# Kernel tuning notes

Measured on AMD Instinct MI355X. Metric: run time of the kernel, lower is better.

## Reference

```python
import jax, jax.numpy as jnp
import numpy as np

# Winograd F(2x2, 3x3) transform matrices
B = jnp.array([[1.0, 0.0, 0.0, 0.0],
               [0.0, 1.0, -1.0, 1.0],
               [-1.0, 1.0, 1.0, 0.0],
               [0.0, 0.0, 0.0, -1.0]], dtype=jnp.float32)
G = jnp.array([[1.0, 0.0, 0.0],
               [0.5, 0.5, 0.5],
               [0.5, -0.5, 0.5],
               [0.0, 0.0, 1.0]], dtype=jnp.float32)
A = jnp.array([[1.0, 0.0],
               [1.0, 1.0],
               [1.0, -1.0],
               [0.0, -1.0]], dtype=jnp.float32)

PADDING = 1


def setup_inputs() -> dict:
    key = jax.random.key(0)
    k1, k2 = jax.random.split(key)
    x = jax.random.normal(k1, (16, 128, 56, 56), dtype=jnp.float32)
    kernel = jax.random.normal(k2, (128, 128, 3, 3), dtype=jnp.float32) * 0.05
    return {"x": x, "kernel": kernel}


def _winograd_fwd(x, kernel):
    # Pad input
    x = jnp.pad(x, ((0, 0), (0, 0), (PADDING, PADDING), (PADDING, PADDING)))
    N, C, H, W = x.shape
    a, overlap, m = 4, 2, 2  # tile size, stride, output tile
    Th = (H - a) // overlap + 1
    Tw = (W - a) // overlap + 1
    H_out, W_out = H - 2, W - 2

    # Filter transform: U = G @ g @ G^T  -> (K, C, 4, 4)
    U = jnp.einsum('ij,kcjl,ml->kcim', G, kernel, G)

    # Extract overlapping 4x4 tiles with stride 2: (N, C, Th, Tw, 4, 4)
    ii = (jnp.arange(Th) * overlap)[:, None] + jnp.arange(a)[None, :]  # (Th, 4)
    jj = (jnp.arange(Tw) * overlap)[:, None] + jnp.arange(a)[None, :]  # (Tw, 4)
    d = x[:, :, ii]               # (N, C, Th, 4, W)
    d = d[:, :, :, :, jj]         # (N, C, Th, 4, Tw, 4)
    d = d.transpose(0, 1, 2, 4, 3, 5)  # (N, C, Th, Tw, 4, 4)

    # Input transform: V = B^T @ d @ B
    V = jnp.einsum('ji,nchwjk,kl->nchwil', B, d, B)  # (N, C, Th, Tw, 4, 4)

    # Elementwise multiply + channel reduction: (N, K, Th, Tw, 4, 4)
    M = jnp.einsum('kcij,nchwij->nkhwij', U, V)

    # Output transform: Y_tile = A^T @ M @ A -> (N, K, Th, Tw, 2, 2)
    Yt = jnp.einsum('ji,nkhwjl,lm->nkhwim', A, M, A)

    # Reassemble tiles into (N, K, H_out, W_out)
    Y = Yt.transpose(0, 1, 2, 4, 3, 5).reshape(N, Yt.shape[1], H_out, W_out)
    return Y


def reference(x, kernel):
    return _winograd_fwd(x, kernel)
```

## Files before the change

### kernel.cpp

```cpp
#include <hip/hip_runtime.h>
#include <hip/hip_bf16.h>

typedef __attribute__((ext_vector_type(8))) short bf16x8;
typedef __attribute__((ext_vector_type(4))) float f32x4;

#define CC 128
#define KK 128
#define HH 56
#define WW 56
#define HW (HH * WW)

#define XP_OFF (512 * 1024)

__device__ __forceinline__ unsigned short f2bf(float f) {
  unsigned int u = __builtin_bit_cast(unsigned int, f);
  u += 0x7FFFu + ((u >> 16) & 1u);
  return (unsigned short)(u >> 16);
}

__device__ __forceinline__ void gload_lds16(const void* g, void* l) {
  __builtin_amdgcn_global_load_lds((__attribute__((address_space(1))) void*)g,
                                   (__attribute__((address_space(3))) void*)l,
                                   16, 0, 0);
}

__global__ void prepack_kernel(const float* __restrict__ x,
                               unsigned short* __restrict__ xp) {
  int idx = blockIdx.x * 256 + threadIdx.x;
  int w = idx % 66;
  int q = idx / 66;
  int cp = q & 15;
  int r = q >> 4;
  int h = r % 58;
  int n = r / 58;
  bool ok = (h >= 1) && (h <= 56) && (w >= 1) && (w <= 56);
  const float* src = x + ((size_t)(n * CC + cp * 8) * HH + (h - 1)) * WW + (w - 1);
  unsigned short o[8];
#pragma unroll
  for (int ci = 0; ci < 8; ++ci) {
    float v = ok ? src[(size_t)ci * HW] : 0.f;
    o[ci] = f2bf(v);
  }
  *(bf16x8*)(xp + (size_t)idx * 8) = *(bf16x8*)o;
}

__global__ void wtrans_kernel(const float* __restrict__ kin,
                              unsigned short* __restrict__ wt) {
  int e = blockIdx.x * 256 + threadIdx.x;
  int j = e & 7;
  int k = (e >> 3) & 127;
  int part = (e >> 10) & 3;
  int step = e >> 12;
  int rs = step >> 2;
  int cs = step & 3;
  int c = cs * 32 + part * 8 + j;
  wt[e] = f2bf(kin[(k * CC + c) * 9 + rs]);
}

__global__ __launch_bounds__(256, 3) void conv_kernel(
    const unsigned short* __restrict__ xp, const unsigned short* __restrict__ wt,
    float* __restrict__ out) {
  __shared__ __align__(16) unsigned char xs[3 * 16384];

  const int tid = threadIdx.x;
  const int lane = tid & 63;
  const int wv = tid >> 6;
  const int wm = wv >> 1;
  const int wn = wv & 1;

  const int wg = ((blockIdx.x & 7) * 56) + (blockIdx.x >> 3);
  const int n = wg / 28;
  const int hp = wg - n * 28;
  const int h0 = hp * 2;

  const unsigned char* xpb = (const unsigned char*)xp;
  const unsigned char* wtb = (const unsigned char*)wt;

  auto issue = [&](int t, int wr) {
    const int rs = t >> 2;
    const int cs = t & 3;
    const int fr = (rs * 11) >> 5;
    const int fs = rs - fr * 3;
    unsigned char* dst = xs + wr * 16384;
    const size_t rowcell = ((size_t)(n * 58 + h0 + fr) * 16 + cs * 4 + wv) * 66 + fs;
    gload_lds16(xpb + (rowcell + lane) * 16, dst + wv * 2048 + lane * 16);
    gload_lds16(xpb + (rowcell + 16 * 66 + lane) * 16,
                dst + wv * 2048 + 1024 + lane * 16);
    const unsigned char* bs = wtb + (size_t)t * 8192 + wv * 2048 + lane * 16;
    gload_lds16(bs, dst + 8192 + wv * 2048 + lane * 16);
    gload_lds16(bs + 1024, dst + 8192 + wv * 2048 + 1024 + lane * 16);
  };

  issue(0, 0);
  issue(1, 1);

  f32x4 acc[4][4] = {};
  const int fo = (lane >> 4) * 2048 + (lane & 15) * 16;

  int rd = 0, wr = 2;
#pragma unroll 1
  for (int t = 0; t < 36; ++t) {
    if (t < 35)
      asm volatile("s_waitcnt vmcnt(4)" ::: "memory");
    else
      asm volatile("s_waitcnt vmcnt(0)" ::: "memory");
    __builtin_amdgcn_s_barrier();

    if (t < 34) issue(t + 2, wr);

    const unsigned char* buf = xs + rd * 16384;
    bf16x8 Af[4], Bf[4];
#pragma unroll
    for (int am = 0; am < 4; ++am)
      Af[am] = *(const bf16x8*)(buf + fo + (wm * 64 + am * 16) * 16);
#pragma unroll
    for (int bn = 0; bn < 4; ++bn)
      Bf[bn] = *(const bf16x8*)(buf + 8192 + fo + (wn * 64 + bn * 16) * 16);

    __builtin_amdgcn_s_setprio(1);
#pragma unroll
    for (int am = 0; am < 4; ++am)
#pragma unroll
      for (int bn = 0; bn < 4; ++bn)
        acc[am][bn] = __builtin_amdgcn_mfma_f32_16x16x32_bf16(
            Af[am], Bf[bn], acc[am][bn], 0, 0, 0);
    __builtin_amdgcn_s_setprio(0);

    rd = (rd == 2) ? 0 : rd + 1;
    wr = (wr == 2) ? 0 : wr + 1;
  }

  const int h = h0 + wm;
  const int q4 = (lane >> 4) << 2;
#pragma unroll
  for (int am = 0; am < 4; ++am) {
    const int w0 = am * 16 + q4;
    if (w0 < WW) {
#pragma unroll
      for (int bn = 0; bn < 4; ++bn) {
        const int k = wn * 64 + bn * 16 + (lane & 15);
        float* op = out + ((size_t)(n * KK + k) * HH + h) * WW + w0;
        *(f32x4*)op = acc[am][bn];
      }
    }
  }
}

extern "C" void kernel_launch(void* const* d_in, const int* in_sizes, int n_in,
                              void* d_out, int out_size, void* d_ws, size_t ws_size,
                              hipStream_t stream) {
  const float* x = (const float*)d_in[0];
  const float* kin = (const float*)d_in[1];
  float* out = (float*)d_out;
  unsigned short* wt = (unsigned short*)d_ws;
  unsigned short* xp = (unsigned short*)((char*)d_ws + XP_OFF);

  hipLaunchKernelGGL(prepack_kernel, dim3(3828), dim3(256), 0, stream, x, xp);
  hipLaunchKernelGGL(wtrans_kernel, dim3(576), dim3(256), 0, stream, kin, wt);
  hipLaunchKernelGGL(conv_kernel, dim3(448), dim3(256), 0, stream, xp, wt, out);
}
```

Measured before the change: 40.33 us.

## Split conv tiles by output-channel half, pack two rows into M, merge prep kernels

The conv workgroup drops from 4 waves to 2 and covers 64 output channels instead of 128. Its 128-row M tile now packs both output rows (112 pixels) instead of padding each row to 64, so fewer MFMA rows are wasted, and the grid doubles to 896 blocks. The LDS pipeline moves from 3 to 4 stages with 3 loads in flight and smaller buffers. The input prepack and weight transform are merged into one launch to save a kernel launch. The risks are duplicated activation loads across the two channel halves and fewer waves per block to hide latency.

```diff
diff --git a/kernel.cpp b/kernel.cpp
--- a/kernel.cpp
+++ b/kernel.cpp
@@ -11,6 +11,8 @@
 #define HW (HH * WW)
 
 #define XP_OFF (512 * 1024)
+#define BUFSZ 12288
+#define ROWB (16 * 66 * 16)
 
 __device__ __forceinline__ unsigned short f2bf(float f) {
   unsigned int u = __builtin_bit_cast(unsigned int, f);
@@ -24,98 +26,117 @@
                                    16, 0, 0);
 }
 
-__global__ void prepack_kernel(const float* __restrict__ x,
-                               unsigned short* __restrict__ xp) {
-  int idx = blockIdx.x * 256 + threadIdx.x;
-  int w = idx % 66;
-  int q = idx / 66;
-  int cp = q & 15;
-  int r = q >> 4;
-  int h = r % 58;
-  int n = r / 58;
-  bool ok = (h >= 1) && (h <= 56) && (w >= 1) && (w <= 56);
-  const float* src = x + ((size_t)(n * CC + cp * 8) * HH + (h - 1)) * WW + (w - 1);
-  unsigned short o[8];
+__global__ void prep_kernel(const float* __restrict__ x,
+                            const float* __restrict__ kin,
+                            unsigned short* __restrict__ xp,
+                            unsigned short* __restrict__ wt) {
+  int b = blockIdx.x;
+  if (b < 3828) {
+    int idx = b * 256 + threadIdx.x;
+    int w = idx % 66;
+    int q = idx / 66;
+    int cp = q & 15;
+    int r = q >> 4;
+    int h = r % 58;
+    int n = r / 58;
+    bool ok = (h >= 1) && (h <= 56) && (w >= 1) && (w <= 56);
+    const float* src =
+        x + ((size_t)(n * CC + cp * 8) * HH + (h - 1)) * WW + (w - 1);
+    unsigned short o[8];
 #pragma unroll
-  for (int ci = 0; ci < 8; ++ci) {
-    float v = ok ? src[(size_t)ci * HW] : 0.f;
-    o[ci] = f2bf(v);
+    for (int ci = 0; ci < 8; ++ci) {
+      float v = ok ? src[(size_t)ci * HW] : 0.f;
+      o[ci] = f2bf(v);
+    }
+    *(bf16x8*)(xp + (size_t)idx * 8) = *(bf16x8*)o;
+  } else {
+    int e = (b - 3828) * 256 + threadIdx.x;
+    int j = e & 7;
+    int l = (e >> 3) & 63;
+    int p = (e >> 9) & 3;
+    int kn = (e >> 11) & 1;
+    int t = e >> 12;
+    int rs = t >> 2;
+    int cs = t & 3;
+    int k = kn * 64 + l;
+    int c = cs * 32 + p * 8 + j;
+    wt[e] = f2bf(kin[(k * CC + c) * 9 + rs]);
   }
-  *(bf16x8*)(xp + (size_t)idx * 8) = *(bf16x8*)o;
 }
 
-__global__ void wtrans_kernel(const float* __restrict__ kin,
-                              unsigned short* __restrict__ wt) {
-  int e = blockIdx.x * 256 + threadIdx.x;
-  int j = e & 7;
-  int k = (e >> 3) & 127;
-  int part = (e >> 10) & 3;
-  int step = e >> 12;
-  int rs = step >> 2;
-  int cs = step & 3;
-  int c = cs * 32 + part * 8 + j;
-  wt[e] = f2bf(kin[(k * CC + c) * 9 + rs]);
-}
-
-__global__ __launch_bounds__(256, 3) void conv_kernel(
+__global__ __launch_bounds__(128, 2) void conv_kernel(
     const unsigned short* __restrict__ xp, const unsigned short* __restrict__ wt,
     float* __restrict__ out) {
-  __shared__ __align__(16) unsigned char xs[3 * 16384];
+  __shared__ __align__(16) unsigned char xs[4 * BUFSZ];
 
   const int tid = threadIdx.x;
   const int lane = tid & 63;
   const int wv = tid >> 6;
-  const int wm = wv >> 1;
-  const int wn = wv & 1;
 
-  const int wg = ((blockIdx.x & 7) * 56) + (blockIdx.x >> 3);
-  const int n = wg / 28;
-  const int hp = wg - n * 28;
+  const int b = blockIdx.x;
+  const int wg = (b & 7) * 112 + (b >> 3);
+  const int kn = wg & 1;
+  const int mh = wg >> 1;
+  const int hp = mh % 28;
+  const int n = mh / 28;
   const int h0 = hp * 2;
 
   const unsigned char* xpb = (const unsigned char*)xp;
   const unsigned char* wtb = (const unsigned char*)wt;
 
-  auto issue = [&](int t, int wr) {
+  int offA0, offA1;
+  {
+    int dr = (lane >= 56) ? 1 : 0;
+    offA0 = dr * ROWB + (lane - 56 * dr) * 16;
+    offA1 = (lane < 48) ? (ROWB + (8 + lane) * 16)
+                        : (57 * 16);
+  }
+
+  auto issue = [&](int t, unsigned char* dst) {
     const int rs = t >> 2;
     const int cs = t & 3;
     const int fr = (rs * 11) >> 5;
     const int fs = rs - fr * 3;
-    unsigned char* dst = xs + wr * 16384;
-    const size_t rowcell = ((size_t)(n * 58 + h0 + fr) * 16 + cs * 4 + wv) * 66 + fs;
-    gload_lds16(xpb + (rowcell + lane) * 16, dst + wv * 2048 + lane * 16);
-    gload_lds16(xpb + (rowcell + 16 * 66 + lane) * 16,
-                dst + wv * 2048 + 1024 + lane * 16);
-    const unsigned char* bs = wtb + (size_t)t * 8192 + wv * 2048 + lane * 16;
-    gload_lds16(bs, dst + 8192 + wv * 2048 + lane * 16);
-    gload_lds16(bs + 1024, dst + 8192 + wv * 2048 + 1024 + lane * 16);
+#pragma unroll
+    for (int pi = 0; pi < 2; ++pi) {
+      const int p = wv * 2 + pi;
+      const size_t ab =
+          (((size_t)(n * 58 + h0 + fr) * 16 + (cs * 4 + p)) * 66 + fs) * 16;
+      gload_lds16(xpb + ab + offA0, dst + p * 2048 + lane * 16);
+      gload_lds16(xpb + ab + offA1, dst + p * 2048 + 1024 + lane * 16);
+      gload_lds16(wtb + (((t * 2 + kn) * 4 + p) << 10) + lane * 16,
+                  dst + 8192 + p * 1024 + lane * 16);
+    }
   };
 
-  issue(0, 0);
-  issue(1, 1);
+  issue(0, xs);
+  issue(1, xs + BUFSZ);
+  issue(2, xs + 2 * BUFSZ);
 
   f32x4 acc[4][4] = {};
   const int fo = (lane >> 4) * 2048 + (lane & 15) * 16;
+  const int fob = (lane >> 4) * 1024 + (lane & 15) * 16;
 
-  int rd = 0, wr = 2;
 #pragma unroll 1
   for (int t = 0; t < 36; ++t) {
-    if (t < 35)
-      asm volatile("s_waitcnt vmcnt(4)" ::: "memory");
+    if (t < 34)
+      asm volatile("s_waitcnt vmcnt(12)" ::: "memory");
+    else if (t == 34)
+      asm volatile("s_waitcnt vmcnt(6)" ::: "memory");
     else
       asm volatile("s_waitcnt vmcnt(0)" ::: "memory");
     __builtin_amdgcn_s_barrier();
 
-    if (t < 34) issue(t + 2, wr);
+    if (t < 33) issue(t + 3, xs + ((t + 3) & 3) * BUFSZ);
 
-    const unsigned char* buf = xs + rd * 16384;
+    const unsigned char* buf = xs + (t & 3) * BUFSZ;
     bf16x8 Af[4], Bf[4];
 #pragma unroll
     for (int am = 0; am < 4; ++am)
-      Af[am] = *(const bf16x8*)(buf + fo + (wm * 64 + am * 16) * 16);
+      Af[am] = *(const bf16x8*)(buf + fo + (wv * 64 + am * 16) * 16);
 #pragma unroll
     for (int bn = 0; bn < 4; ++bn)
-      Bf[bn] = *(const bf16x8*)(buf + 8192 + fo + (wn * 64 + bn * 16) * 16);
+      Bf[bn] = *(const bf16x8*)(buf + 8192 + fob + bn * 16 * 16);
 
     __builtin_amdgcn_s_setprio(1);
 #pragma unroll
@@ -125,20 +146,19 @@
         acc[am][bn] = __builtin_amdgcn_mfma_f32_16x16x32_bf16(
             Af[am], Bf[bn], acc[am][bn], 0, 0, 0);
     __builtin_amdgcn_s_setprio(0);
-
-    rd = (rd == 2) ? 0 : rd + 1;
-    wr = (wr == 2) ? 0 : wr + 1;
   }
 
-  const int h = h0 + wm;
   const int q4 = (lane >> 4) << 2;
 #pragma unroll
   for (int am = 0; am < 4; ++am) {
-    const int w0 = am * 16 + q4;
-    if (w0 < WW) {
+    const int pxb = wv * 64 + am * 16 + q4;
+    if (pxb < 112) {
+      const int dr = (pxb >= 56) ? 1 : 0;
+      const int w0 = pxb - 56 * dr;
+      const int h = h0 + dr;
 #pragma unroll
       for (int bn = 0; bn < 4; ++bn) {
-        const int k = wn * 64 + bn * 16 + (lane & 15);
+        const int k = kn * 64 + bn * 16 + (lane & 15);
         float* op = out + ((size_t)(n * KK + k) * HH + h) * WW + w0;
         *(f32x4*)op = acc[am][bn];
       }
@@ -155,7 +175,6 @@
   unsigned short* wt = (unsigned short*)d_ws;
   unsigned short* xp = (unsigned short*)((char*)d_ws + XP_OFF);
 
-  hipLaunchKernelGGL(prepack_kernel, dim3(3828), dim3(256), 0, stream, x, xp);
-  hipLaunchKernelGGL(wtrans_kernel, dim3(576), dim3(256), 0, stream, kin, wt);
-  hipLaunchKernelGGL(conv_kernel, dim3(448), dim3(256), 0, stream, xp, wt, out);
+  hipLaunchKernelGGL(prep_kernel, dim3(4404), dim3(256), 0, stream, x, kin, xp, wt);
+  hipLaunchKernelGGL(conv_kernel, dim3(896), dim3(128), 0, stream, xp, wt, out);
 }
```

Result: slower. 48.29 us (+19.7%).
